# Kernel optimization log

Hardware: AMD Instinct MI355X
Metric: run time of the kernel (lower is better)

The kernel has to match this reference:

```python
import jax, jax.numpy as jnp
import numpy as np
import math

B, N, D_IN, D_OUT = 8, 2048, 128, 128
NEG_BIG = -10000.0

def setup_inputs() -> dict:
    key = jax.random.key(0)
    k_in, k_adj, kq, kk, kv, kbq, kbk, kbv = jax.random.split(key, 8)
    scale = 1.0 / math.sqrt(D_IN)
    inputs = jax.random.normal(k_in, (B, N, D_IN), dtype=jnp.float32)
    adj = jax.random.randint(k_adj, (B, N, N), 0, 2, dtype=jnp.int32)
    Wq = jax.random.uniform(kq, (D_IN, D_OUT), jnp.float32, -scale, scale)
    Wk = jax.random.uniform(kk, (D_IN, D_OUT), jnp.float32, -scale, scale)
    Wv = jax.random.uniform(kv, (D_IN, D_OUT), jnp.float32, -scale, scale)
    bq = jax.random.uniform(kbq, (D_OUT,), jnp.float32, -scale, scale)
    bk = jax.random.uniform(kbk, (D_OUT,), jnp.float32, -scale, scale)
    bv = jax.random.uniform(kbv, (D_OUT,), jnp.float32, -scale, scale)
    return {"inputs": inputs, "adj": adj, "Wq": Wq, "bq": bq,
            "Wk": Wk, "bk": bk, "Wv": Wv, "bv": bv}

def reference(inputs, adj, Wq, bq, Wk, bk, Wv, bv):
    # QKV projections: [B, N, D_OUT]
    q = inputs @ Wq + bq
    k = inputs @ Wk + bk
    v = inputs @ Wv + bv
    # additive adjacency bias: 0 where edge, -10000 where no edge
    bias = (1.0 - adj.astype(jnp.float32)) * NEG_BIG
    # scaled dot-product scores [B, N, N]
    a = jnp.einsum('bnd,bmd->bnm', q, k) / jnp.sqrt(jnp.float32(q.shape[-1]))
    a = a + bias
    p = jax.nn.softmax(a, axis=-1)  # dropout_prob=0.0 -> identity
    h = jnp.einsum('bnm,bmd->bnd', p, v)
    return jax.nn.elu(h)
```

## Files before the change

kernel.cpp:

```cpp
#include <hip/hip_runtime.h>

typedef unsigned short u16;
typedef __bf16 bf16x8 __attribute__((ext_vector_type(8)));
typedef float  fx4    __attribute__((ext_vector_type(4)));

__device__ __forceinline__ u16 f2bf(float f) {
    unsigned int x = __builtin_bit_cast(unsigned int, f);
    x = x + 0x7fffu + ((x >> 16) & 1u);
    return (u16)(x >> 16);
}
__device__ __forceinline__ __bf16 f2bf16(float f) {
    return __builtin_bit_cast(__bf16, f2bf(f));
}

#define MFMA16(a, b, c) __builtin_amdgcn_mfma_f32_16x16x32_bf16((a), (b), (c), 0, 0, 0)
#define WAVE_LDS_SYNC() __asm__ volatile("s_waitcnt lgkmcnt(0)" ::: "memory")

__global__ __launch_bounds__(256) void wt_kernel(
    const float* __restrict__ Wq, const float* __restrict__ Wk,
    const float* __restrict__ Wv, u16* __restrict__ WT)
{
    const int o = blockIdx.x * 256 + threadIdx.x;
    const int p = o >> 14, rem = o & 16383, c = rem >> 7, k = rem & 127;
    const float* W = (p == 0) ? Wq : ((p == 1) ? Wk : Wv);
    WT[o] = f2bf(W[k * 128 + c]);
}

__global__ __launch_bounds__(256, 2) void qkv_kernel(
    const float* __restrict__ X, const u16* __restrict__ WT,
    const float* __restrict__ bq, const float* __restrict__ bk,
    const float* __restrict__ bv,
    u16* __restrict__ Qf, u16* __restrict__ Kf, u16* __restrict__ Vf)
{
    __shared__ __align__(16) u16 tb[4][2048];

    const int tid  = threadIdx.x;
    const int w    = tid >> 6;
    const int lane = tid & 63;
    const int n    = lane & 15;
    const int quad = lane >> 4;
    const int gw   = blockIdx.x * 4 + w;
    const int rt   = gw >> 1, ch = gw & 1;
    const int row0 = rt * 16;
    const int b    = row0 >> 11;
    const int keyb = row0 & 2047;
    u16* tbuf = tb[w];

    bf16x8 af[4];
    {
        const float* xr = X + (size_t)(row0 + n) * 128;
#pragma unroll
        for (int kk = 0; kk < 4; ++kk) {
            float4 f0 = *(const float4*)(xr + kk * 32 + quad * 8);
            float4 f1 = *(const float4*)(xr + kk * 32 + quad * 8 + 4);
            bf16x8 a;
            a[0] = f2bf16(f0.x); a[1] = f2bf16(f0.y); a[2] = f2bf16(f0.z); a[3] = f2bf16(f0.w);
            a[4] = f2bf16(f1.x); a[5] = f2bf16(f1.y); a[6] = f2bf16(f1.z); a[7] = f2bf16(f1.w);
            af[kk] = a;
        }
    }

    const float* Bs[2] = {bq, bk};
#pragma unroll
    for (int p = 0; p < 2; ++p) {
        const u16* wt = WT + p * 16384;
#pragma unroll
        for (int nt = 0; nt < 4; ++nt) {
            const int col0 = ch * 64 + nt * 16;
            fx4 acc = {0.f, 0.f, 0.f, 0.f};
#pragma unroll
            for (int kk = 0; kk < 4; ++kk) {
                bf16x8 bf = __builtin_bit_cast(bf16x8,
                    *(const uint4*)&wt[(col0 + n) * 128 + kk * 32 + quad * 8]);
                acc = MFMA16(af[kk], bf, acc);
            }
            const float bb = Bs[p][col0 + n];
#pragma unroll
            for (int r = 0; r < 4; ++r)
                tbuf[(quad * 4 + r) * 72 + nt * 16 + n] = f2bf(acc[r] + bb);
        }
        WAVE_LDS_SYNC();
#pragma unroll
        for (int kkl = 0; kkl < 2; ++kkl) {
            const int kk = ch * 2 + kkl;
            uint4 frag = *(const uint4*)&tbuf[n * 72 + kkl * 32 + quad * 8];
            u16* dst;
            if (p == 0)
                dst = Qf + (((size_t)(b * 128 + (keyb >> 4)) * 4 + kk) << 9);
            else
                dst = Kf + ((((size_t)(b * 64 + (keyb >> 5)) * 2 + ((keyb >> 4) & 1)) * 4 + kk) << 9);
            *(uint4*)(dst + lane * 8) = frag;
        }
        WAVE_LDS_SYNC();
    }

    {
        const u16* wtv = WT + 2 * 16384;
#pragma unroll
        for (int d0 = 0; d0 < 4; ++d0) {
            const int dbase = ch * 64 + d0 * 16;
            fx4 acc = {0.f, 0.f, 0.f, 0.f};
#pragma unroll
            for (int kk = 0; kk < 4; ++kk) {
                bf16x8 wf = __builtin_bit_cast(bf16x8,
                    *(const uint4*)&wtv[(dbase + n) * 128 + kk * 32 + quad * 8]);
                acc = MFMA16(wf, af[kk], acc);
            }
#pragma unroll
            for (int r = 0; r < 4; ++r)
                tbuf[(d0 * 16 + quad * 4 + r) * 20 + n] = f2bf(acc[r] + bv[dbase + quad * 4 + r]);
        }
        WAVE_LDS_SYNC();
        const int t = keyb >> 5, half = (keyb >> 4) & 1;
        const int n2 = lane & 15, quadh = (lane >> 4) & 1, g = lane >> 5;
#pragma unroll
        for (int dtl = 0; dtl < 2; ++dtl) {
            const int dl = dtl * 2 + g;
            uint4 frag = *(const uint4*)&tbuf[(dl * 16 + n2) * 20 + quadh * 8];
            const int dt = ch * 4 + dl;
            u16* dv = Vf + (((size_t)(b * 64 + t) * 8 + dt) << 9)
                         + half * 256 + (lane & 31) * 8;
            *(uint4*)dv = frag;
        }
    }
}

__global__ __launch_bounds__(256, 4) void attn_kernel(
    const u16* __restrict__ Qf, const u16* __restrict__ Kf,
    const u16* __restrict__ Vf, const int* __restrict__ adj,
    float* __restrict__ out)
{
    __shared__ __align__(16) float mO[4][16 * 128];
    __shared__ __align__(16) float ml[4][16];
    __shared__ __align__(16) u16 pl[4][640];

    const int tid  = threadIdx.x;
    const int h    = tid >> 6;
    const int lane = tid & 63;
    const int n    = lane & 15;
    const int quad = lane >> 4;
    const int b    = blockIdx.x & 7;
    const int qt   = blockIdx.x >> 3;
    const int q0   = qt * 16;
    const size_t bN = (size_t)b * 2048;

    bf16x8 qf[4];
    {
        const u16* qp = Qf + ((size_t)(b * 128 + qt) << 11) + lane * 8;
#pragma unroll
        for (int kk = 0; kk < 4; ++kk)
            qf[kk] = __builtin_bit_cast(bf16x8, *(const uint4*)(qp + (kk << 9)));
    }
    const u16* Kb = Kf + ((size_t)b << 18);
    const u16* Vb = Vf + ((size_t)b << 18);

    bf16x8 ones;
#pragma unroll
    for (int j = 0; j < 8; ++j) ones[j] = f2bf16(1.0f);

    fx4 O[8];
#pragma unroll
    for (int i = 0; i < 8; ++i) O[i] = (fx4){0.f, 0.f, 0.f, 0.f};
    fx4 Lacc = {0.f, 0.f, 0.f, 0.f};

    const int* adjb = adj + (bN + q0 + quad * 4) * 2048;
    const float SCALE = 0.08838834764831845f;
    u16* pw = pl[h];

    int a0c[4], a1c[4];
    {
        const int k0 = h * 512;
#pragma unroll
        for (int r = 0; r < 4; ++r) {
            a0c[r] = adjb[(size_t)r * 2048 + k0 + n];
            a1c[r] = adjb[(size_t)r * 2048 + k0 + 16 + n];
        }
    }

    for (int t = 0; t < 16; ++t) {
        const int tg = h * 16 + t;
        const u16* kt_ = Kb + ((size_t)tg << 12) + lane * 8;
        const u16* vt_ = Vb + ((size_t)tg << 12) + lane * 8;

        int a0n[4], a1n[4];
        if (t < 15) {
            const int kn = h * 512 + (t + 1) * 32;
#pragma unroll
            for (int r = 0; r < 4; ++r) {
                a0n[r] = adjb[(size_t)r * 2048 + kn + n];
                a1n[r] = adjb[(size_t)r * 2048 + kn + 16 + n];
            }
        }

        fx4 S0 = {0.f, 0.f, 0.f, 0.f}, S1 = {0.f, 0.f, 0.f, 0.f};
#pragma unroll
        for (int kk = 0; kk < 4; ++kk) {
            bf16x8 kb0 = __builtin_bit_cast(bf16x8, *(const uint4*)(kt_ + (kk << 9)));
            bf16x8 kb1 = __builtin_bit_cast(bf16x8, *(const uint4*)(kt_ + ((4 + kk) << 9)));
            S0 = MFMA16(qf[kk], kb0, S0);
            S1 = MFMA16(qf[kk], kb1, S1);
        }

#pragma unroll
        for (int r = 0; r < 4; ++r) {
            const float p0 = a0c[r] ? __expf(S0[r] * SCALE) : 0.f;
            const float p1 = a1c[r] ? __expf(S1[r] * SCALE) : 0.f;
            pw[(quad * 4 + r) * 40 + n]      = f2bf(p0);
            pw[(quad * 4 + r) * 40 + 16 + n] = f2bf(p1);
        }
#pragma unroll
        for (int r = 0; r < 4; ++r) { a0c[r] = a0n[r]; a1c[r] = a1n[r]; }

        WAVE_LDS_SYNC();
        bf16x8 pf = __builtin_bit_cast(bf16x8, *(const uint4*)&pw[n * 40 + quad * 8]);

#pragma unroll
        for (int dt = 0; dt < 8; ++dt) {
            bf16x8 vf = __builtin_bit_cast(bf16x8, *(const uint4*)(vt_ + (dt << 9)));
            O[dt] = MFMA16(pf, vf, O[dt]);
        }
        Lacc = MFMA16(pf, ones, Lacc);
    }

#pragma unroll
    for (int r = 0; r < 4; ++r) {
        const int row = quad * 4 + r;
        if (n == 0) ml[h][row] = Lacc[r];
#pragma unroll
        for (int dt = 0; dt < 8; ++dt)
            mO[h][row * 128 + dt * 16 + n] = O[dt][r];
    }
    __syncthreads();

#pragma unroll
    for (int r = 0; r < 4; ++r) {
        const int row = quad * 4 + r;
        const float L = ml[0][row] + ml[1][row] + ml[2][row] + ml[3][row];
        const float linv = 1.f / L;
        float* po = out + (bN + q0 + row) * 128;
#pragma unroll
        for (int dti = 0; dti < 2; ++dti) {
            const int dt = h * 2 + dti;
            float o = 0.f;
#pragma unroll
            for (int g = 0; g < 4; ++g) o += mO[g][row * 128 + dt * 16 + n];
            const float hh = o * linv;
            po[dt * 16 + n] = (hh > 0.f) ? hh : (__expf(hh) - 1.f);
        }
    }
}

extern "C" void kernel_launch(void* const* d_in, const int* in_sizes, int n_in,
                              void* d_out, int out_size, void* d_ws, size_t ws_size,
                              hipStream_t stream) {
    (void)in_sizes; (void)n_in; (void)out_size; (void)ws_size;
    const float* X   = (const float*)d_in[0];
    const int*   adj = (const int*)d_in[1];
    const float* Wq  = (const float*)d_in[2];
    const float* bq  = (const float*)d_in[3];
    const float* Wk  = (const float*)d_in[4];
    const float* bk  = (const float*)d_in[5];
    const float* Wv  = (const float*)d_in[6];
    const float* bv  = (const float*)d_in[7];
    float* out = (float*)d_out;

    u16* WT  = (u16*)d_out;
    u16* Qf  = (u16*)d_ws;
    u16* Kf  = Qf + (size_t)16384 * 128;
    u16* Vf  = Kf + (size_t)16384 * 128;

    wt_kernel<<<192, 256, 0, stream>>>(Wq, Wk, Wv, WT);
    qkv_kernel<<<512, 256, 0, stream>>>(X, WT, bq, bk, bv, Qf, Kf, Vf);
    attn_kernel<<<1024, 256, 0, stream>>>(Qf, Kf, Vf, adj, out);
}
```

Baseline: 275.4 us.

## Reduce attention partials via LDS atomics to shrink shared memory and double occupancy

Replaces the per-wave partial output buffers (4x16x128 floats) with a single shared accumulator that each wave adds into with LDS atomicAdd, cutting shared memory by roughly 4x. Launch bounds are raised to 8 blocks per SIMD-group target so more workgroups can be resident and hide the latency of the adjacency and K/V loads. The cost is an extra zero-init pass plus a barrier, and contended float atomics in LDS during the final reduction. Tighter register limits could also cause spills.

```diff
diff --git a/kernel.cpp b/kernel.cpp
--- a/kernel.cpp
+++ b/kernel.cpp
@@ -125,13 +125,13 @@
     }
 }
 
-__global__ __launch_bounds__(256, 4) void attn_kernel(
+__global__ __launch_bounds__(256, 8) void attn_kernel(
     const u16* __restrict__ Qf, const u16* __restrict__ Kf,
     const u16* __restrict__ Vf, const int* __restrict__ adj,
     float* __restrict__ out)
 {
-    __shared__ __align__(16) float mO[4][16 * 128];
-    __shared__ __align__(16) float ml[4][16];
+    __shared__ __align__(16) float accO[16 * 128];
+    __shared__ __align__(16) float accL[16];
     __shared__ __align__(16) u16 pl[4][640];
 
     const int tid  = threadIdx.x;
@@ -144,6 +144,9 @@
     const int q0   = qt * 16;
     const size_t bN = (size_t)b * 2048;
 
+    for (int i = tid; i < 16 * 128; i += 256) accO[i] = 0.f;
+    if (tid < 16) accL[tid] = 0.f;
+
     bf16x8 qf[4];
     {
         const u16* qp = Qf + ((size_t)(b * 128 + qt) << 11) + lane * 8;
@@ -166,6 +169,8 @@
     const int* adjb = adj + (bN + q0 + quad * 4) * 2048;
     const float SCALE = 0.08838834764831845f;
     u16* pw = pl[h];
+
+    __syncthreads();
 
     int a0c[4], a1c[4];
     {
@@ -223,30 +228,21 @@
     }
 
 #pragma unroll
-    for (int r = 0; r < 4; ++r) {
-        const int row = quad * 4 + r;
-        if (n == 0) ml[h][row] = Lacc[r];
-#pragma unroll
-        for (int dt = 0; dt < 8; ++dt)
-            mO[h][row * 128 + dt * 16 + n] = O[dt][r];
+    for (int dt = 0; dt < 8; ++dt) {
+#pragma unroll
+        for (int r = 0; r < 4; ++r)
+            atomicAdd(&accO[(quad * 4 + r) * 128 + dt * 16 + n], O[dt][r]);
+    }
+    if (n == 0) {
+#pragma unroll
+        for (int r = 0; r < 4; ++r) atomicAdd(&accL[quad * 4 + r], Lacc[r]);
     }
     __syncthreads();
 
-#pragma unroll
-    for (int r = 0; r < 4; ++r) {
-        const int row = quad * 4 + r;
-        const float L = ml[0][row] + ml[1][row] + ml[2][row] + ml[3][row];
-        const float linv = 1.f / L;
-        float* po = out + (bN + q0 + row) * 128;
-#pragma unroll
-        for (int dti = 0; dti < 2; ++dti) {
-            const int dt = h * 2 + dti;
-            float o = 0.f;
-#pragma unroll
-            for (int g = 0; g < 4; ++g) o += mO[g][row * 128 + dt * 16 + n];
-            const float hh = o * linv;
-            po[dt * 16 + n] = (hh > 0.f) ? hh : (__expf(hh) - 1.f);
-        }
+    for (int i = tid; i < 16 * 128; i += 256) {
+        const int row = i >> 7;
+        const float hh = accO[i] / accL[row];
+        out[(bN + q0 + row) * 128 + (i & 127)] = (hh > 0.f) ? hh : (__expf(hh) - 1.f);
     }
 }
 
```

Result: slower. 418.5 us (+51.9%).
